# Kernel tuning notes

Measured on AMD Instinct MI355X. Metric: run time of the kernel, lower is better.

Reference implementation:

```python
import jax, jax.numpy as jnp
import numpy as np


def setup_inputs() -> dict:
    key = jax.random.key(0)
    k1, k2, k3, k4 = jax.random.split(key, 4)
    b, h, w, c, ns = 1, 256, 256, 128, 8
    L = h * w
    win = (h // ns) * (w // ns)
    return {
        "q": jax.random.normal(k1, (b, L, c), jnp.float32),
        "k": jax.random.normal(k2, (b, L, c), jnp.float32),
        "v": jax.random.normal(k3, (b, L, c), jnp.float32),
        "attn_mask": jax.random.normal(k4, (ns * ns, win, win), jnp.float32),
        "num_splits": 8,
        "with_shift": 1,
        "h": 256,
        "w": 256,
    }


def reference(q, k, v, attn_mask, num_splits, with_shift, h, w):
    b, L, c = q.shape
    ns = num_splits
    wh, ww = h // ns, w // ns
    scale = c ** 0.5

    q4 = q.reshape(b, h, w, c)
    k4 = k.reshape(b, h, w, c)
    v4 = v.reshape(b, h, w, c)

    if with_shift:
        sh, sw = wh // 2, ww // 2
        # NOTE: source rolls dims=(2,3) of the (b,h,w,c) view -> shifts W and C axes.
        roll_fwd = lambda x: jnp.roll(x, (-sh, -sw), axis=(2, 3))
        q4, k4, v4 = roll_fwd(q4), roll_fwd(k4), roll_fwd(v4)

    def split(x):  # (b,h,w,c) -> (b, ns*ns, wh*ww, c)
        x = x.reshape(b, ns, wh, ns, ww, c)
        return x.transpose(0, 1, 3, 2, 4, 5).reshape(b, ns * ns, wh * ww, c)

    qw, kw, vw = split(q4), split(k4), split(v4)

    scores = jnp.einsum("bnqc,bnkc->bnqk", qw, kw) / scale  # (b, ns^2, L_w, L_w)
    if with_shift:
        scores = scores + attn_mask[None]  # attn_mask.repeat(b,1,1), b==1
    attn = jax.nn.softmax(scores, axis=-1)
    out = jnp.einsum("bnqk,bnkc->bnqc", attn, vw)

    # merge windows back: (b, ns*ns, wh*ww, c) -> (b, h, w, c)
    out = out.reshape(b, ns, ns, wh, ww, c).transpose(0, 1, 3, 2, 4, 5).reshape(b, h, w, c)
    if with_shift:
        out = jnp.roll(out, (sh, sw), axis=(2, 3))
    return out.reshape(b, h * w, c)
```

## Files before the change

### kernel.cpp

```cpp
#include <hip/hip_runtime.h>
#include <hip/hip_bf16.h>


typedef __attribute__((ext_vector_type(8))) short bhalf8;
typedef __attribute__((ext_vector_type(4))) float f4;
typedef __attribute__((ext_vector_type(4))) int i4;

#define MFMA16(a, b, c) __builtin_amdgcn_mfma_f32_16x16x32_bf16((a), (b), (c), 0, 0, 0)

__device__ __forceinline__ unsigned short f2bf(float f) {
    unsigned u = __builtin_bit_cast(unsigned, f);
    return (unsigned short)((u + 0x7fffu + ((u >> 16) & 1u)) >> 16);
}

__device__ __forceinline__ int rowOff(int i, int j, int r) {
    int y = i * 32 + (r >> 5);
    int x = (j * 32 + (r & 31) + 16) & 255;
    return ((y << 8) + x) << 7;
}

__global__ __launch_bounds__(256, 2)
void swin_attn_kernel(const float* __restrict__ Qg, const float* __restrict__ Kg,
                      const float* __restrict__ Vg, const float* __restrict__ Mg,
                      float* __restrict__ Og) {
    __shared__ __align__(16) unsigned char smem[49152];

    const int tid  = threadIdx.x;
    const int lane = tid & 63;
    const int wv   = tid >> 6;
    const int l15  = lane & 15;
    const int l4   = lane >> 4;

    const int g     = blockIdx.x;
    const int w_idx = (g & 7) + ((g >> 6) << 3);
    const int tq    = (g >> 3) & 7;
    const int wi = w_idx >> 3, wj = w_idx & 7;
    const int q0 = tq * 128;

    const float SCALE = 11.313708498984760f;
    const float K1    = 1.4426950408889634f / SCALE;

    {
        const int rl  = tid >> 4;
        const int ch0 = (tid & 15) * 8;
#pragma unroll
        for (int p = 0; p < 8; ++p) {
            int row = p * 16 + rl;
            const float* src = Qg + rowOff(wi, wj, q0 + row) + ch0;
            f4 a = *(const f4*)src;
            f4 b = *(const f4*)(src + 4);
            union { unsigned short us[8]; i4 v; } pk;
#pragma unroll
            for (int u = 0; u < 4; ++u) { pk.us[u] = f2bf(a[u]); pk.us[u + 4] = f2bf(b[u]); }
            *(i4*)(smem + row * 256 + ((ch0 * 2) ^ ((row & 7) << 4))) = pk.v;
        }
    }
    __syncthreads();

    bhalf8 qf[2][4];
#pragma unroll
    for (int qb = 0; qb < 2; ++qb)
#pragma unroll
        for (int ks = 0; ks < 4; ++ks) {
            int row = wv * 32 + qb * 16 + l15;
            qf[qb][ks] = *(const bhalf8*)(smem + row * 256 + ((ks * 64 + l4 * 16) ^ ((row & 7) << 4)));
        }
    __syncthreads();

    f4 Oacc[2][8];
#pragma unroll
    for (int qb = 0; qb < 2; ++qb)
#pragma unroll
        for (int cf = 0; cf < 8; ++cf) Oacc[qb][cf] = (f4){0.f, 0.f, 0.f, 0.f};
    float lpart[8] = {0.f, 0.f, 0.f, 0.f, 0.f, 0.f, 0.f, 0.f};

    unsigned char* Plds = smem + 32768 + wv * 4096;
    const float* mrow = Mg + ((size_t)w_idx << 20);

    for (int kv = 0; kv < 16; ++kv) {
        const int s0 = kv * 64;

        f4 acc[2][4];
#pragma unroll
        for (int qb = 0; qb < 2; ++qb)
#pragma unroll
            for (int sf = 0; sf < 4; ++sf) {
                int qrow = q0 + wv * 32 + qb * 16 + l4 * 4;
                const float* mp = mrow + (size_t)qrow * 1024 + (s0 + sf * 16 + l15);
                f4 t;
                t[0] = mp[0] * SCALE; t[1] = mp[1024] * SCALE;
                t[2] = mp[2048] * SCALE; t[3] = mp[3072] * SCALE;
                acc[qb][sf] = t;
            }

        {
            const int rl  = tid >> 4;
            const int ch0 = (tid & 15) * 8;
#pragma unroll
            for (int p = 0; p < 4; ++p) {
                int row = p * 16 + rl;
                const float* src = Kg + rowOff(wi, wj, s0 + row) + ch0;
                f4 a = *(const f4*)src;
                f4 b = *(const f4*)(src + 4);
                union { unsigned short us[8]; i4 v; } pk;
#pragma unroll
                for (int u = 0; u < 4; ++u) { pk.us[u] = f2bf(a[u]); pk.us[u + 4] = f2bf(b[u]); }
                *(i4*)(smem + row * 256 + ((ch0 * 2) ^ ((row & 7) << 4))) = pk.v;
            }
#pragma unroll
            for (int p = 0; p < 4; ++p) {
                int task = tid + p * 256;
                int ch = task & 127;
                int sb = task >> 7;
                union { unsigned short us[8]; i4 v; } pk;
#pragma unroll
                for (int u = 0; u < 8; ++u)
                    pk.us[u] = f2bf(Vg[rowOff(wi, wj, s0 + sb * 8 + u) + ch]);
                *(i4*)(smem + 16384 + ch * 128 + ((sb * 16) ^ ((ch & 7) << 4))) = pk.v;
            }
        }
        __syncthreads();

#pragma unroll
        for (int sf = 0; sf < 4; ++sf) {
            int row = sf * 16 + l15;
            const unsigned char* rb = smem + row * 256;
#pragma unroll
            for (int ks = 0; ks < 4; ++ks) {
                bhalf8 kb = *(const bhalf8*)(rb + ((ks * 64 + l4 * 16) ^ ((row & 7) << 4)));
                acc[0][sf] = MFMA16(qf[0][ks], kb, acc[0][sf]);
                acc[1][sf] = MFMA16(qf[1][ks], kb, acc[1][sf]);
            }
        }

#pragma unroll
        for (int qb = 0; qb < 2; ++qb)
#pragma unroll
            for (int sf = 0; sf < 4; ++sf)
#pragma unroll
                for (int r = 0; r < 4; ++r) {
                    float p = __builtin_amdgcn_exp2f(acc[qb][sf][r] * K1);
                    lpart[qb * 4 + r] += p;
                    int q = qb * 16 + l4 * 4 + r;
                    int s = sf * 16 + l15;
                    *(unsigned short*)(Plds + q * 128 + ((s * 2) ^ ((q & 7) << 4))) = f2bf(p);
                }

        bhalf8 pa[2][2];
#pragma unroll
        for (int qb = 0; qb < 2; ++qb)
#pragma unroll
            for (int ks = 0; ks < 2; ++ks) {
                int q = qb * 16 + l15;
                pa[qb][ks] = *(const bhalf8*)(Plds + q * 128 + ((ks * 64 + l4 * 16) ^ ((q & 7) << 4)));
            }
#pragma unroll
        for (int cf = 0; cf < 8; ++cf) {
            int row = cf * 16 + l15;
            const unsigned char* rb = smem + 16384 + row * 128;
#pragma unroll
            for (int ks = 0; ks < 2; ++ks) {
                bhalf8 vb = *(const bhalf8*)(rb + ((ks * 64 + l4 * 16) ^ ((row & 7) << 4)));
                Oacc[0][cf] = MFMA16(pa[0][ks], vb, Oacc[0][cf]);
                Oacc[1][cf] = MFMA16(pa[1][ks], vb, Oacc[1][cf]);
            }
        }
        __syncthreads();
    }

#pragma unroll
    for (int t = 0; t < 8; ++t) {
        float v = lpart[t];
        v += __shfl_xor(v, 1); v += __shfl_xor(v, 2);
        v += __shfl_xor(v, 4); v += __shfl_xor(v, 8);
        lpart[t] = 1.0f / v;
    }

#pragma unroll
    for (int qb = 0; qb < 2; ++qb)
#pragma unroll
        for (int r = 0; r < 4; ++r) {
            int rg = q0 + wv * 32 + qb * 16 + l4 * 4 + r;
            float* dst = Og + rowOff(wi, wj, rg);
            float rin = lpart[qb * 4 + r];
#pragma unroll
            for (int cf = 0; cf < 8; ++cf)
                dst[cf * 16 + l15] = Oacc[qb][cf][r] * rin;
        }
}

extern "C" void kernel_launch(void* const* d_in, const int* in_sizes, int n_in,
                              void* d_out, int out_size, void* d_ws, size_t ws_size,
                              hipStream_t stream) {
    const float* q = (const float*)d_in[0];
    const float* k = (const float*)d_in[1];
    const float* v = (const float*)d_in[2];
    const float* m = (const float*)d_in[3];
    float* out = (float*)d_out;
    hipLaunchKernelGGL(swin_attn_kernel, dim3(512), dim3(256), 0, stream, q, k, v, m, out);
}
```

Before: 467.4 us.

## Use 8 waves per block and prefetch next mask tile into registers

Doubles the block to 512 threads so each wave owns 16 query rows instead of 32, halving per-wave accumulator state and raising occupancy. It also software-pipelines the attention-mask load by fetching the next KV tile's mask values into a second register buffer before the current tile's compute, using a two-step unrolled loop. The aim is to hide global mask latency, which is the dominant memory stream. The cost is that the K/V fills per block are now shared across more waves, with more barrier participants and more registers for the double-buffered mask.

```diff
diff --git a/kernel.cpp b/kernel.cpp
--- a/kernel.cpp
+++ b/kernel.cpp
@@ -19,7 +19,85 @@
     return ((y << 8) + x) << 7;
 }
 
-__global__ __launch_bounds__(256, 2)
+#define MLOAD(MN, S0) do {                                                    \
+    const float* mp_ = mrow + (S0) + l15;                                     \
+    _Pragma("unroll") for (int sf_ = 0; sf_ < 4; ++sf_)                       \
+        _Pragma("unroll") for (int r_ = 0; r_ < 4; ++r_)                      \
+            MN[sf_ * 4 + r_] = mp_[r_ * 1024 + sf_ * 16];                     \
+} while (0)
+
+#define BODY(KV, MC, MN) do {                                                 \
+    const int s0 = (KV) * 64;                                                 \
+          \
+    MLOAD(MN, (((KV) + 1) & 15) * 64);                                        \
+                       \
+    {                                                                         \
+        const int rl = tid >> 4, ch0 = (tid & 15) * 8;                        \
+        _Pragma("unroll") for (int p = 0; p < 2; ++p) {                       \
+            int row = p * 32 + rl;                                            \
+            const float* src = Kg + rowOff(wi, wj, s0 + row) + ch0;           \
+            f4 a = *(const f4*)src;                                           \
+            f4 b = *(const f4*)(src + 4);                                     \
+            union { unsigned short us[8]; i4 v; } pk;                         \
+            _Pragma("unroll") for (int u = 0; u < 4; ++u) {                   \
+                pk.us[u] = f2bf(a[u]); pk.us[u + 4] = f2bf(b[u]); }           \
+            *(i4*)(smem + row * 256 + ((ch0 * 2) ^ ((row & 7) << 4))) = pk.v; \
+        }                                                                     \
+                      \
+        _Pragma("unroll") for (int p = 0; p < 2; ++p) {                       \
+            int task = tid + p * 512;                                         \
+            int ch = task & 127, sb = task >> 7;                              \
+            union { unsigned short us[8]; i4 v; } pk;                         \
+            _Pragma("unroll") for (int u = 0; u < 8; ++u)                     \
+                pk.us[u] = f2bf(Vg[rowOff(wi, wj, s0 + sb * 8 + u) + ch]);    \
+            *(i4*)(smem + 16384 + ch * 128 + ((sb * 16) ^ ((ch & 7) << 4))) = pk.v; \
+        }                                                                     \
+    }                                                                         \
+    __syncthreads();                                                          \
+        \
+    f4 acc[4];                                                                \
+    _Pragma("unroll") for (int sf = 0; sf < 4; ++sf) {                        \
+        f4 t;                                                                 \
+        t[0] = MC[sf * 4 + 0] * SCALE; t[1] = MC[sf * 4 + 1] * SCALE;         \
+        t[2] = MC[sf * 4 + 2] * SCALE; t[3] = MC[sf * 4 + 3] * SCALE;         \
+        acc[sf] = t;                                                          \
+    }                                                                         \
+                                  \
+    _Pragma("unroll") for (int sf = 0; sf < 4; ++sf) {                        \
+        int row = sf * 16 + l15;                                              \
+        const unsigned char* rb = smem + row * 256;                           \
+        _Pragma("unroll") for (int ks = 0; ks < 4; ++ks) {                    \
+            bhalf8 kb = *(const bhalf8*)(rb + ((ks * 64 + l4 * 16) ^ ((row & 7) << 4))); \
+            acc[sf] = MFMA16(qf[ks], kb, acc[sf]);                            \
+        }                                                                     \
+    }                                                                         \
+       \
+    _Pragma("unroll") for (int sf = 0; sf < 4; ++sf)                          \
+        _Pragma("unroll") for (int r = 0; r < 4; ++r) {                       \
+            float p = __builtin_amdgcn_exp2f(acc[sf][r] * K1);                \
+            lpart[r] += p;                                                    \
+            int q = l4 * 4 + r, s = sf * 16 + l15;                            \
+            *(unsigned short*)(Plds + q * 128 + ((s * 2) ^ ((q & 7) << 4))) = f2bf(p); \
+        }                                                                     \
+                                                      \
+    bhalf8 pa[2];                                                             \
+    {                                                                         \
+        int q = l15;                                                          \
+        _Pragma("unroll") for (int ks = 0; ks < 2; ++ks)                      \
+            pa[ks] = *(const bhalf8*)(Plds + q * 128 + ((ks * 64 + l4 * 16) ^ ((q & 7) << 4))); \
+    }                                                                         \
+    _Pragma("unroll") for (int cf = 0; cf < 8; ++cf) {                        \
+        int row = cf * 16 + l15;                                              \
+        const unsigned char* rb = smem + 16384 + row * 128;                   \
+        _Pragma("unroll") for (int ks = 0; ks < 2; ++ks) {                    \
+            bhalf8 vb = *(const bhalf8*)(rb + ((ks * 64 + l4 * 16) ^ ((row & 7) << 4))); \
+            Oacc[cf] = MFMA16(pa[ks], vb, Oacc[cf]);                          \
+        }                                                                     \
+    }                                                                         \
+    __syncthreads();                                                          \
+} while (0)
+
+__global__ __launch_bounds__(512, 4)
 void swin_attn_kernel(const float* __restrict__ Qg, const float* __restrict__ Kg,
                       const float* __restrict__ Vg, const float* __restrict__ Mg,
                       float* __restrict__ Og) {
@@ -44,8 +122,8 @@
         const int rl  = tid >> 4;
         const int ch0 = (tid & 15) * 8;
 #pragma unroll
-        for (int p = 0; p < 8; ++p) {
-            int row = p * 16 + rl;
+        for (int p = 0; p < 4; ++p) {
+            int row = p * 32 + rl;
             const float* src = Qg + rowOff(wi, wj, q0 + row) + ch0;
             f4 a = *(const f4*)src;
             f4 b = *(const f4*)(src + 4);
@@ -57,119 +135,33 @@
     }
     __syncthreads();
 
-    bhalf8 qf[2][4];
+    bhalf8 qf[4];
+    {
+        int row = wv * 16 + l15;
 #pragma unroll
-    for (int qb = 0; qb < 2; ++qb)
-#pragma unroll
-        for (int ks = 0; ks < 4; ++ks) {
-            int row = wv * 32 + qb * 16 + l15;
-            qf[qb][ks] = *(const bhalf8*)(smem + row * 256 + ((ks * 64 + l4 * 16) ^ ((row & 7) << 4)));
-        }
+        for (int ks = 0; ks < 4; ++ks)
+            qf[ks] = *(const bhalf8*)(smem + row * 256 + ((ks * 64 + l4 * 16) ^ ((row & 7) << 4)));
+    }
     __syncthreads();
 
-    f4 Oacc[2][8];
+    f4 Oacc[8];
 #pragma unroll
-    for (int qb = 0; qb < 2; ++qb)
-#pragma unroll
-        for (int cf = 0; cf < 8; ++cf) Oacc[qb][cf] = (f4){0.f, 0.f, 0.f, 0.f};
-    float lpart[8] = {0.f, 0.f, 0.f, 0.f, 0.f, 0.f, 0.f, 0.f};
+    for (int cf = 0; cf < 8; ++cf) Oacc[cf] = (f4){0.f, 0.f, 0.f, 0.f};
+    float lpart[4] = {0.f, 0.f, 0.f, 0.f};
 
-    unsigned char* Plds = smem + 32768 + wv * 4096;
-    const float* mrow = Mg + ((size_t)w_idx << 20);
+    unsigned char* Plds = smem + 32768 + wv * 2048;
+    const float* mrow = Mg + ((size_t)w_idx << 20) + (size_t)(q0 + wv * 16 + l4 * 4) * 1024;
 
-    for (int kv = 0; kv < 16; ++kv) {
-        const int s0 = kv * 64;
+    float mA[16], mB[16];
+    MLOAD(mA, 0);
 
-        f4 acc[2][4];
-#pragma unroll
-        for (int qb = 0; qb < 2; ++qb)
-#pragma unroll
-            for (int sf = 0; sf < 4; ++sf) {
-                int qrow = q0 + wv * 32 + qb * 16 + l4 * 4;
-                const float* mp = mrow + (size_t)qrow * 1024 + (s0 + sf * 16 + l15);
-                f4 t;
-                t[0] = mp[0] * SCALE; t[1] = mp[1024] * SCALE;
-                t[2] = mp[2048] * SCALE; t[3] = mp[3072] * SCALE;
-                acc[qb][sf] = t;
-            }
-
-        {
-            const int rl  = tid >> 4;
-            const int ch0 = (tid & 15) * 8;
-#pragma unroll
-            for (int p = 0; p < 4; ++p) {
-                int row = p * 16 + rl;
-                const float* src = Kg + rowOff(wi, wj, s0 + row) + ch0;
-                f4 a = *(const f4*)src;
-                f4 b = *(const f4*)(src + 4);
-                union { unsigned short us[8]; i4 v; } pk;
-#pragma unroll
-                for (int u = 0; u < 4; ++u) { pk.us[u] = f2bf(a[u]); pk.us[u + 4] = f2bf(b[u]); }
-                *(i4*)(smem + row * 256 + ((ch0 * 2) ^ ((row & 7) << 4))) = pk.v;
-            }
-#pragma unroll
-            for (int p = 0; p < 4; ++p) {
-                int task = tid + p * 256;
-                int ch = task & 127;
-                int sb = task >> 7;
-                union { unsigned short us[8]; i4 v; } pk;
-#pragma unroll
-                for (int u = 0; u < 8; ++u)
-                    pk.us[u] = f2bf(Vg[rowOff(wi, wj, s0 + sb * 8 + u) + ch]);
-                *(i4*)(smem + 16384 + ch * 128 + ((sb * 16) ^ ((ch & 7) << 4))) = pk.v;
-            }
-        }
-        __syncthreads();
-
-#pragma unroll
-        for (int sf = 0; sf < 4; ++sf) {
-            int row = sf * 16 + l15;
-            const unsigned char* rb = smem + row * 256;
-#pragma unroll
-            for (int ks = 0; ks < 4; ++ks) {
-                bhalf8 kb = *(const bhalf8*)(rb + ((ks * 64 + l4 * 16) ^ ((row & 7) << 4)));
-                acc[0][sf] = MFMA16(qf[0][ks], kb, acc[0][sf]);
-                acc[1][sf] = MFMA16(qf[1][ks], kb, acc[1][sf]);
-            }
-        }
-
-#pragma unroll
-        for (int qb = 0; qb < 2; ++qb)
-#pragma unroll
-            for (int sf = 0; sf < 4; ++sf)
-#pragma unroll
-                for (int r = 0; r < 4; ++r) {
-                    float p = __builtin_amdgcn_exp2f(acc[qb][sf][r] * K1);
-                    lpart[qb * 4 + r] += p;
-                    int q = qb * 16 + l4 * 4 + r;
-                    int s = sf * 16 + l15;
-                    *(unsigned short*)(Plds + q * 128 + ((s * 2) ^ ((q & 7) << 4))) = f2bf(p);
-                }
-
-        bhalf8 pa[2][2];
-#pragma unroll
-        for (int qb = 0; qb < 2; ++qb)
-#pragma unroll
-            for (int ks = 0; ks < 2; ++ks) {
-                int q = qb * 16 + l15;
-                pa[qb][ks] = *(const bhalf8*)(Plds + q * 128 + ((ks * 64 + l4 * 16) ^ ((q & 7) << 4)));
-            }
-#pragma unroll
-        for (int cf = 0; cf < 8; ++cf) {
-            int row = cf * 16 + l15;
-            const unsigned char* rb = smem + 16384 + row * 128;
-#pragma unroll
-            for (int ks = 0; ks < 2; ++ks) {
-                bhalf8 vb = *(const bhalf8*)(rb + ((ks * 64 + l4 * 16) ^ ((row & 7) << 4)));
-                Oacc[0][cf] = MFMA16(pa[0][ks], vb, Oacc[0][cf]);
-                Oacc[1][cf] = MFMA16(pa[1][ks], vb, Oacc[1][cf]);
-            }
-        }
-        __syncthreads();
+    for (int kv2 = 0; kv2 < 16; kv2 += 2) {
+        BODY(kv2, mA, mB);
+        BODY(kv2 + 1, mB, mA);
     }
 
 #pragma unroll
-    for (int t = 0; t < 8; ++t) {
+    for (int t = 0; t < 4; ++t) {
         float v = lpart[t];
         v += __shfl_xor(v, 1); v += __shfl_xor(v, 2);
         v += __shfl_xor(v, 4); v += __shfl_xor(v, 8);
@@ -177,16 +169,14 @@
     }
 
 #pragma unroll
-    for (int qb = 0; qb < 2; ++qb)
+    for (int r = 0; r < 4; ++r) {
+        int rg = q0 + wv * 16 + l4 * 4 + r;
+        float* dst = Og + rowOff(wi, wj, rg);
+        float rin = lpart[r];
 #pragma unroll
-        for (int r = 0; r < 4; ++r) {
-            int rg = q0 + wv * 32 + qb * 16 + l4 * 4 + r;
-            float* dst = Og + rowOff(wi, wj, rg);
-            float rin = lpart[qb * 4 + r];
-#pragma unroll
-            for (int cf = 0; cf < 8; ++cf)
-                dst[cf * 16 + l15] = Oacc[qb][cf][r] * rin;
-        }
+        for (int cf = 0; cf < 8; ++cf)
+            dst[cf * 16 + l15] = Oacc[cf][r] * rin;
+    }
 }
 
 extern "C" void kernel_launch(void* const* d_in, const int* in_sizes, int n_in,
@@ -197,5 +187,5 @@
     const float* v = (const float*)d_in[2];
     const float* m = (const float*)d_in[3];
     float* out = (float*)d_out;
-    hipLaunchKernelGGL(swin_attn_kernel, dim3(512), dim3(256), 0, stream, q, k, v, m, out);
+    hipLaunchKernelGGL(swin_attn_kernel, dim3(512), dim3(512), 0, stream, q, k, v, m, out);
 }
```

After: 771.7 us. +65.1%, slower.
